# Kernel tuning notes

Hardware: AMD Instinct MI355X
Metric: run time of the kernel (lower is better)

## Reference

```python
import jax, jax.numpy as jnp
import numpy as np

B, S_SRC, S_TRG = 128, 512, 128
VIN, VOUT = 128, 128
E, H = 128, 256          # embed, encoder hidden
HD = 2 * H               # decoder hidden = 512 (concat of bi-dir encoder states)
DENC = 2 * H             # encoder output feature dim = 512


def setup_inputs() -> dict:
    key = jax.random.key(0)
    ks = jax.random.split(key, 20)
    g = lambda k, shape: (jax.random.normal(k, shape, jnp.float32) * 0.05)
    inp = {
        "src": jax.random.randint(ks[0], (B, S_SRC), 0, VIN, jnp.int32),
        "trg": jax.random.randint(ks[1], (B, S_TRG), 0, VOUT, jnp.int32),
        # encoder
        "enc_emb": g(ks[2], (VIN, E)),
        "enc_Wih_f": g(ks[3], (4 * H, E)),
        "enc_Whh_f": g(ks[4], (4 * H, H)),
        "enc_b_f": g(ks[5], (4 * H,)),
        "enc_Wih_b": g(ks[6], (4 * H, E)),
        "enc_Whh_b": g(ks[7], (4 * H, H)),
        "enc_b_b": g(ks[8], (4 * H,)),
        # decoder
        "dec_emb": g(ks[9], (VOUT, E)),
        "dec_Wih": g(ks[10], (4 * HD, E + DENC)),
        "dec_Whh": g(ks[11], (4 * HD, HD)),
        "dec_b": g(ks[12], (4 * HD,)),
        # attention: Linear(dec_hid + enc_dim -> HD), v: Linear(HD -> 1)
        "attn_W": g(ks[13], (HD + DENC, HD)),
        "attn_b": g(ks[14], (HD,)),
        "attn_v": g(ks[15], (HD,)),
        # output projection
        "out_W": g(ks[16], (HD, VOUT)),
        "out_b": g(ks[17], (VOUT,)),
    }
    return inp


def _lstm_cell(h, c, x, Wih, Whh, b):
    gates = x @ Wih.T + h @ Whh.T + b               # [B, 4H]
    i, f, gg, o = jnp.split(gates, 4, axis=-1)       # PyTorch gate order i,f,g,o
    i, f, o = jax.nn.sigmoid(i), jax.nn.sigmoid(f), jax.nn.sigmoid(o)
    c = f * c + i * jnp.tanh(gg)
    h = o * jnp.tanh(c)
    return h, c


def _lstm_scan(xs, Wih, Whh, b, reverse=False):
    # xs: [S, B, E] -> hs: [S, B, H] (time-aligned), plus final (h, c)
    Bn, Hn = xs.shape[1], Whh.shape[1]
    init = (jnp.zeros((Bn, Hn), xs.dtype), jnp.zeros((Bn, Hn), xs.dtype))
    def step(carry, x):
        h, c = _lstm_cell(carry[0], carry[1], x, Wih, Whh, b)
        return (h, c), h
    (h, c), hs = jax.lax.scan(step, init, xs, reverse=reverse)
    return hs, h, c


def reference(src, trg, enc_emb, enc_Wih_f, enc_Whh_f, enc_b_f,
              enc_Wih_b, enc_Whh_b, enc_b_b, dec_emb, dec_Wih, dec_Whh,
              dec_b, attn_W, attn_b, attn_v, out_W, out_b):
    # ----- encoder (bidirectional LSTM) -----
    emb = enc_emb[src]                                # [B, S, E]
    xs = jnp.swapaxes(emb, 0, 1)                      # [S, B, E]
    hs_f, hf, cf = _lstm_scan(xs, enc_Wih_f, enc_Whh_f, enc_b_f, reverse=False)
    hs_b, hb, cb = _lstm_scan(xs, enc_Wih_b, enc_Whh_b, enc_b_b, reverse=True)
    enc_out = jnp.swapaxes(jnp.concatenate([hs_f, hs_b], -1), 0, 1)  # [B, S, 2H]
    hidden = jnp.concatenate([hf, hb], -1)            # [B, HD]  (hidden.view(1,B,-1))
    cell = jnp.concatenate([cf, cb], -1)              # [B, HD]

    # attention linear split: energy = tanh([h, enc] @ W + b)
    Wh, We = attn_W[:HD], attn_W[HD:]
    enc_proj = jnp.einsum("bsd,de->bse", enc_out, We)  # [B, S, HD] precomputed

    def dec_step(carry, tok):
        h, c = carry
        e = jnp.tanh(h[:, None, :] @ Wh + enc_proj + attn_b)     # [B, S, HD]
        scores = jnp.einsum("bse,e->bs", e, attn_v)              # [B, S]
        aw = jax.nn.softmax(scores, axis=1)
        ctx = jnp.einsum("bs,bsd->bd", aw, enc_out)              # [B, DENC]
        x = jnp.concatenate([dec_emb[tok], ctx], -1)             # [B, E+DENC]
        h, c = _lstm_cell(h, c, x, dec_Wih, dec_Whh, dec_b)
        logits = h @ out_W + out_b                               # [B, VOUT]
        return (h, c), logits

    # teacher forcing (ratio=1.0): input at step t is trg[:, t-1], t = 1..T-1
    toks = jnp.swapaxes(trg[:, :-1], 0, 1)            # [T-1, B]
    _, logits = jax.lax.scan(dec_step, (hidden, cell), toks)
    logits = jnp.swapaxes(logits, 0, 1)               # [B, T-1, VOUT]
    outputs = jnp.concatenate(
        [jnp.zeros((src.shape[0], 1, VOUT), logits.dtype), logits], axis=1)
    return outputs
```

## Files before the change

kernel.cpp:

```cpp
#include <hip/hip_runtime.h>


typedef _Float16 f16;
typedef _Float16 half8 __attribute__((ext_vector_type(8)));
typedef float f32x4 __attribute__((ext_vector_type(4)));
typedef char char8v __attribute__((ext_vector_type(8)));

#define MFMA16(a, b, c) __builtin_amdgcn_mfma_f32_16x16x32_f16((a), (b), (c), 0, 0, 0)

#define PSCALE (2.5f / 127.f)
#define PINV   (127.f / 2.5f)

__device__ __forceinline__ float fsig(float x) {
    return __builtin_amdgcn_rcpf(1.f + __expf(-x));
}
__device__ __forceinline__ float ftanh(float x) {
    return 1.f - 2.f * __builtin_amdgcn_rcpf(1.f + __expf(2.f * x));
}
__device__ __forceinline__ int frag_idx(int m, int k, int KS) {
    return (((m >> 4) * KS + (k >> 5)) * 64 + (((k >> 3) & 3) * 16 + (m & 15))) * 8 + (k & 7);
}

__device__ __forceinline__ void lds_barrier() {
    asm volatile("s_waitcnt lgkmcnt(0)" ::: "memory");
    __builtin_amdgcn_sched_barrier(0);
    __builtin_amdgcn_s_barrier();
    __builtin_amdgcn_sched_barrier(0);
}

__global__ void k_zero(unsigned* __restrict__ s)
{
    for (int z = threadIdx.x; z < 4112; z += 256) s[z] = 0u;
}

__global__ __launch_bounds__(256) void k_prep(
    const float* __restrict__ attn_W, const float* __restrict__ out_W,
    const float* __restrict__ enc_emb,
    const float* __restrict__ wihf, const float* __restrict__ wihb,
    const float* __restrict__ whhf, const float* __restrict__ whhb,
    const float* __restrict__ dec_emb, const float* __restrict__ dec_wih,
    const float* __restrict__ dec_whh,
    f16* __restrict__ WhT_sw, f16* __restrict__ outWT_sw,
    f16* __restrict__ whhf_sw, f16* __restrict__ whhb_sw,
    f16* __restrict__ decwih_sw, f16* __restrict__ decwhh_sw,
    f16* __restrict__ WeT, f16* __restrict__ emb16,
    f16* __restrict__ wihf16, f16* __restrict__ wihb16,
    f16* __restrict__ decemb16, float* __restrict__ out)
{
    long i = (long)blockIdx.x * 256 + threadIdx.x;
    if (i >= 3784704L) return;
    long idx = i;
    if (idx < 262144) {
        int j = idx & 7, lane = (idx >> 3) & 63, c = lane & 15, q = lane >> 4;
        int ks = (idx >> 9) & 15, nt = idx >> 13;
        WhT_sw[idx] = (f16)attn_W[(ks * 32 + q * 8 + j) * 512 + nt * 16 + c];
        return;
    }
    idx -= 262144;
    if (idx < 65536) {
        int j = idx & 7, lane = (idx >> 3) & 63, c = lane & 15, q = lane >> 4;
        int ks = (idx >> 9) & 15, nt = idx >> 13;
        outWT_sw[idx] = (f16)out_W[(ks * 32 + q * 8 + j) * 128 + nt * 16 + c];
        return;
    }
    idx -= 65536;
    if (idx < 262144) {
        int j = idx & 7, lane = (idx >> 3) & 63, c = lane & 15, q = lane >> 4;
        int ks = (idx >> 9) & 7, nt = idx >> 12;
        whhf_sw[idx] = (f16)whhf[(nt * 16 + c) * 256 + ks * 32 + q * 8 + j];
        return;
    }
    idx -= 262144;
    if (idx < 262144) {
        int j = idx & 7, lane = (idx >> 3) & 63, c = lane & 15, q = lane >> 4;
        int ks = (idx >> 9) & 7, nt = idx >> 12;
        whhb_sw[idx] = (f16)whhb[(nt * 16 + c) * 256 + ks * 32 + q * 8 + j];
        return;
    }
    idx -= 262144;
    if (idx < 1310720) {
        int j = idx & 7, lane = (idx >> 3) & 63, c = lane & 15, q = lane >> 4;
        int r2 = idx >> 9; int ks = r2 % 20, nt = r2 / 20;
        decwih_sw[idx] = (f16)dec_wih[(nt * 16 + c) * 640 + ks * 32 + q * 8 + j];
        return;
    }
    idx -= 1310720;
    if (idx < 1048576) {
        int j = idx & 7, lane = (idx >> 3) & 63, c = lane & 15, q = lane >> 4;
        int ks = (idx >> 9) & 15, nt = idx >> 13;
        decwhh_sw[idx] = (f16)dec_whh[(nt * 16 + c) * 512 + ks * 32 + q * 8 + j];
        return;
    }
    idx -= 1048576;
    if (idx < 262144) { int e = idx >> 9, d = idx & 511; WeT[idx] = (f16)attn_W[(512 + d) * 512 + e]; return; }
    idx -= 262144;
    if (idx < 16384)  { emb16[idx] = (f16)enc_emb[idx]; return; }
    idx -= 16384;
    if (idx < 131072) { wihf16[idx] = (f16)wihf[idx]; return; }
    idx -= 131072;
    if (idx < 131072) { wihb16[idx] = (f16)wihb[idx]; return; }
    idx -= 131072;
    if (idx < 16384)  { decemb16[idx] = (f16)dec_emb[idx]; return; }
    idx -= 16384;
    if (idx < 16384)  { int b = idx >> 7, v = idx & 127; out[b * 16384 + v] = 0.f; return; }
}

__global__ __launch_bounds__(256) void k_vocab(
    const f16* __restrict__ emb, const f16* __restrict__ wihf,
    const f16* __restrict__ wihb, const float* __restrict__ bf_,
    const float* __restrict__ bb_, f16* __restrict__ xg_vocab)
{
    int bn = blockIdx.x;
    int tid = threadIdx.x, wave = tid >> 6, lane = tid & 63;
    int col = lane & 15, quad = lane >> 4;
    int wr = wave >> 1, wc = wave & 1;

    f32x4 acc[4][4] = {};
    for (int ks = 0; ks < 4; ++ks) {
        int k0 = ks * 32 + quad * 8;
        half8 a[4], bfr[4];
        for (int i = 0; i < 4; ++i)
            a[i] = *(const half8*)(emb + (wr * 64 + i * 16 + col) * 128 + k0);
        for (int j = 0; j < 4; ++j) {
            int n = bn * 128 + wc * 64 + j * 16 + col;
            const f16* wp = (n < 1024) ? (wihf + n * 128) : (wihb + (n - 1024) * 128);
            bfr[j] = *(const half8*)(wp + k0);
        }
        for (int i = 0; i < 4; ++i)
            for (int j = 0; j < 4; ++j)
                acc[i][j] = MFMA16(a[i], bfr[j], acc[i][j]);
    }
    for (int j = 0; j < 4; ++j) {
        int n = bn * 128 + wc * 64 + j * 16 + col;
        float bias = (n < 1024) ? bf_[n] : bb_[n - 1024];
        for (int i = 0; i < 4; ++i) {
            int vbase = wr * 64 + i * 16 + quad * 4;
            for (int r = 0; r < 4; ++r)
                xg_vocab[(vbase + r) * 2048 + n] = (f16)(acc[i][j][r] + bias);
        }
    }
}

__global__ __launch_bounds__(512, 1) void k_enc(
    const int* __restrict__ src, const f16* __restrict__ xg_vocab,
    const f16* __restrict__ whhf_sw, const f16* __restrict__ whhb_sw,
    f16* __restrict__ enc_out, f16* __restrict__ hdec0, float* __restrict__ c_ws)
{
    int blk = blockIdx.x;
    int dir = blk >> 3, bbase = (blk & 7) * 16;
    int tid = threadIdx.x, wave = tid >> 6, lane = tid & 63;
    int col = lane & 15, quad = lane >> 4;
    const f16* whh = dir ? whhb_sw : whhf_sw;

    __shared__ f16 hb[2][16][264];
    __shared__ f16 xvb[2][16][1032];
    __shared__ unsigned short stall[8192];

    for (int z = tid; z < 2 * 16 * 264; z += 512) ((f16*)hb)[z] = (f16)0.f;
    for (int z = tid; z < 8192; z += 512) stall[z] = (unsigned short)src[bbase * 512 + z];
    float cc[2][4] = {};

    half8 bst[16];
    #pragma unroll
    for (int nt = 0; nt < 2; ++nt)
        #pragma unroll
        for (int kk = 0; kk < 8; ++kk) {
            int tile = wave * 2 + nt;
            bst[nt * 8 + kk] = *(const half8*)(whh + ((tile * 8 + kk) * 64 + lane) * 8);
        }
    __syncthreads();

    int xrow = tid >> 7, xoff = (tid & 127) * 8;
    half8 xr[4];
    {
        int ts0 = dir ? 511 : 0;
        #pragma unroll
        for (int it = 0; it < 4; ++it) {
            int row = it * 4 + xrow;
            int tok = stall[row * 512 + ts0];
            xr[it] = *(const half8*)(xg_vocab + tok * 2048 + dir * 1024 + xoff);
        }
        #pragma unroll
        for (int it = 0; it < 4; ++it)
            *(half8*)(&xvb[0][it * 4 + xrow][xoff]) = xr[it];
    }
    __syncthreads();

    int ts_prev = 0;
    for (int t = 0; t < 512; ++t) {
        int ts = dir ? (511 - t) : t;
        int cur = t & 1, prv = cur ^ 1;

        if (t < 511) {
            int tsn = dir ? (510 - t) : (t + 1);
            #pragma unroll
            for (int it = 0; it < 4; ++it) {
                int row = it * 4 + xrow;
                int tok = stall[row * 512 + tsn];
                xr[it] = *(const half8*)(xg_vocab + tok * 2048 + dir * 1024 + xoff);
            }
        }

        if (t > 0) {
            int b = tid >> 5, seg = tid & 31;
            *(half8*)(enc_out + ((size_t)(bbase + b) * 512 + ts_prev) * 512 + dir * 256 + seg * 8) =
                *(const half8*)(&hb[prv][b][seg * 8]);
        }

        half8 a[8];
        #pragma unroll
        for (int kk = 0; kk < 8; ++kk)
            a[kk] = *(const half8*)(&hb[prv][col][kk * 32 + quad * 8]);

        f32x4 acc[4][2] = {};
        #pragma unroll
        for (int kk = 0; kk < 8; ++kk) {
            half8 bv[6];
            #pragma unroll
            for (int g = 1; g < 4; ++g)
                #pragma unroll
                for (int nt = 0; nt < 2; ++nt) {
                    int tile = g * 16 + wave * 2 + nt;
                    bv[(g - 1) * 2 + nt] =
                        *(const half8*)(whh + ((tile * 8 + kk) * 64 + lane) * 8);
                }
            #pragma unroll
            for (int nt = 0; nt < 2; ++nt)
                acc[0][nt] = MFMA16(a[kk], bst[nt * 8 + kk], acc[0][nt]);
            #pragma unroll
            for (int g = 1; g < 4; ++g)
                #pragma unroll
                for (int nt = 0; nt < 2; ++nt)
                    acc[g][nt] = MFMA16(a[kk], bv[(g - 1) * 2 + nt], acc[g][nt]);
        }

        #pragma unroll
        for (int nt = 0; nt < 2; ++nt) {
            int hcol = wave * 32 + nt * 16 + col;
            #pragma unroll
            for (int r = 0; r < 4; ++r) {
                int b = quad * 4 + r;
                float gi = (float)xvb[cur][b][0 * 256 + hcol] + acc[0][nt][r];
                float gf = (float)xvb[cur][b][1 * 256 + hcol] + acc[1][nt][r];
                float gg = (float)xvb[cur][b][2 * 256 + hcol] + acc[2][nt][r];
                float go = (float)xvb[cur][b][3 * 256 + hcol] + acc[3][nt][r];
                float ig = fsig(gi), fg = fsig(gf), g2 = ftanh(gg), og = fsig(go);
                float cv = fg * cc[nt][r] + ig * g2;
                cc[nt][r] = cv;
                float h = og * ftanh(cv);
                hb[cur][b][hcol] = (f16)h;
            }
        }

        if (t < 511) {
            #pragma unroll
            for (int it = 0; it < 4; ++it)
                *(half8*)(&xvb[prv][it * 4 + xrow][xoff]) = xr[it];
        }

        lds_barrier();
        ts_prev = ts;
    }

    {
        int b = tid >> 5, seg = tid & 31;
        *(half8*)(enc_out + ((size_t)(bbase + b) * 512 + ts_prev) * 512 + dir * 256 + seg * 8) =
            *(const half8*)(&hb[1][b][seg * 8]);
    }
    #pragma unroll
    for (int nt = 0; nt < 2; ++nt) {
        int hcol = wave * 32 + nt * 16 + col;
        #pragma unroll
        for (int r = 0; r < 4; ++r) {
            int b = quad * 4 + r;
            int m = bbase + b, k = dir * 256 + hcol;
            hdec0[frag_idx(m, k, 16)] = hb[1][b][hcol];
            c_ws[m * 512 + k] = cc[nt][r];
        }
    }
}

__global__ __launch_bounds__(256) void k_proj(
    const f16* __restrict__ enc_out, const f16* __restrict__ WeT,
    char* __restrict__ proj8)
{
    int blk = blockIdx.x;
    int bm = blk & 511, bn = blk >> 9;
    int tid = threadIdx.x, wave = tid >> 6, lane = tid & 63;
    int col = lane & 15, quad = lane >> 4;
    int wr = wave >> 1, wc = wave & 1;

    f32x4 acc[4][4] = {};
    for (int ks = 0; ks < 16; ++ks) {
        int k0 = ks * 32 + quad * 8;
        half8 a[4], bfr[4];
        for (int i = 0; i < 4; ++i) {
            int m = bm * 128 + wr * 64 + i * 16 + col;
            a[i] = *(const half8*)(enc_out + (size_t)m * 512 + k0);
        }
        for (int j = 0; j < 4; ++j) {
            int n = bn * 128 + wc * 64 + j * 16 + col;
            bfr[j] = *(const half8*)(WeT + n * 512 + k0);
        }
        for (int i = 0; i < 4; ++i)
            for (int j = 0; j < 4; ++j)
                acc[i][j] = MFMA16(a[i], bfr[j], acc[i][j]);
    }
    for (int j = 0; j < 4; ++j) {
        int n = bn * 128 + wc * 64 + j * 16 + col;
        for (int i = 0; i < 4; ++i) {
            int mbase = bm * 128 + wr * 64 + i * 16 + quad * 4;
            for (int r = 0; r < 4; ++r) {
                float v = acc[i][j][r] * PINV;
                int q = (int)rintf(v);
                q = (q > 127) ? 127 : ((q < -127) ? -127 : q);
                proj8[(size_t)(mbase + r) * 512 + n] = (char)q;
            }
        }
    }
}

__global__ __launch_bounds__(256) void k_qinit(
    const f16* __restrict__ h0_sw, const f16* __restrict__ WhT_sw,
    float* __restrict__ qpart)
{
    int j = blockIdx.x;
    int tid = threadIdx.x, wave = tid >> 6, lane = tid & 63;
    int col = lane & 15, quad = lane >> 4;
    half8 a[2];
    #pragma unroll
    for (int i = 0; i < 2; ++i)
        a[i] = *(const half8*)(h0_sw + (((wave * 2 + i) * 16 + j) * 64 + lane) * 8);
    for (int nt = 0; nt < 32; ++nt) {
        half8 bfr = *(const half8*)(WhT_sw + ((nt * 16 + j) * 64 + lane) * 8);
        f32x4 q0 = {}, q1 = {};
        q0 = MFMA16(a[0], bfr, q0);
        q1 = MFMA16(a[1], bfr, q1);
        #pragma unroll
        for (int r = 0; r < 4; ++r) {
            qpart[(j * 128 + wave * 32 + quad * 4 + r) * 512 + nt * 16 + col] = q0[r];
            qpart[(j * 128 + wave * 32 + 16 + quad * 4 + r) * 512 + nt * 16 + col] = q1[r];
        }
    }
}

__global__ __launch_bounds__(512, 2) void k_step(
    const char* __restrict__ proj8, const f16* __restrict__ enc_out,
    float* __restrict__ qpart, const float* __restrict__ attn_bp,
    const float* __restrict__ attn_vp, const int* __restrict__ trg,
    const f16* __restrict__ dec_emb, f16* __restrict__ x_sw,
    float* __restrict__ part_m, float* __restrict__ part_l,
    float* __restrict__ part_ctx, f16* __restrict__ hdec0,
    f16* __restrict__ hdec1, const f16* __restrict__ wih_sw,
    const f16* __restrict__ whh_sw, const float* __restrict__ dec_bp,
    float* __restrict__ c_ws, f16* __restrict__ hhist_sw,
    const f16* __restrict__ WhT_sw, unsigned* __restrict__ flags, int tt)
{
    int blk = blockIdx.x;
    int tid = threadIdx.x, wave = tid >> 6, lane = tid & 63;
    int col = lane & 15, quad = lane >> 4;

    __shared__ float q[512];
    __shared__ float sc[256];
    __shared__ float ctxred[8][512];
    __shared__ float wred[8], wred2[8];
    __shared__ f16 hsl[64][40];
    __shared__ float gm[64][2];
    __shared__ float gq[4][4][4][64];

    if (blk < 32) {
        int tg = tt - 1;
        if (tg >= 0) {
            int j = blk >> 1, mh = blk & 1;
            if (tid < 64) {
                int bb = mh * 64 + tid;
                float m0 = part_m[bb * 2 + 0], m1 = part_m[bb * 2 + 1];
                float l0 = part_l[bb * 2 + 0], l1 = part_l[bb * 2 + 1];
                float M = fmaxf(m0, m1);
                float g0 = __expf(m0 - M), g1 = __expf(m1 - M);
                float inv = 1.f / (g0 * l0 + g1 * l1);
                gm[tid][0] = g0 * inv;
                gm[tid][1] = g1 * inv;
            }
            __syncthreads();

            for (int io = 0; io < 64; io += 8) {
                float p0[8], p1[8];
                #pragma unroll
                for (int k = 0; k < 8; ++k) {
                    int bb = mh * 64 + io + k;
                    p0[k] = part_ctx[(size_t)(bb * 2 + 0) * 512 + tid];
                    p1[k] = part_ctx[(size_t)(bb * 2 + 1) * 512 + tid];
                }
                #pragma unroll
                for (int k = 0; k < 8; ++k) {
                    int lr = io + k, bb = mh * 64 + lr;
                    x_sw[frag_idx(bb, 128 + tid, 20)] =
                        (f16)(gm[lr][0] * p0[k] + gm[lr][1] * p1[k]);
                }
            }
            __syncthreads();

            const f16* hprev = (tg & 1) ? hdec1 : hdec0;
            f16* hnext = (tg & 1) ? hdec0 : hdec1;

            int h = wave >> 2, mw = wave & 3;
            int mtile = mh * 4 + mw;

            f32x4 acc[4] = {};
            for (int kg = 0; kg < 20; kg += 4) {
                half8 ag[4], bvg[4][4];
                #pragma unroll
                for (int kk = 0; kk < 4; ++kk) {
                    int ks = kg + kk;
                    ag[kk] = *(const half8*)(x_sw + ((mtile * 20 + ks) * 64 + lane) * 8);
                    #pragma unroll
                    for (int q2 = 0; q2 < 4; ++q2) {
                        int jt = h * 4 + q2, g = jt >> 1, u2 = jt & 1;
                        int ntile = g * 32 + j * 2 + u2;
                        bvg[kk][q2] = *(const half8*)(wih_sw + ((ntile * 20 + ks) * 64 + lane) * 8);
                    }
                }
                #pragma unroll
                for (int kk = 0; kk < 4; ++kk)
                    #pragma unroll
                    for (int q2 = 0; q2 < 4; ++q2)
                        acc[q2] = MFMA16(ag[kk], bvg[kk][q2], acc[q2]);
            }
            for (int kg = 0; kg < 16; kg += 4) {
                half8 ag[4], bvg[4][4];
                #pragma unroll
                for (int kk = 0; kk < 4; ++kk) {
                    int ks2 = kg + kk;
                    ag[kk] = *(const half8*)(hprev + ((mtile * 16 + ks2) * 64 + lane) * 8);
                    #pragma unroll
                    for (int q2 = 0; q2 < 4; ++q2) {
                        int jt = h * 4 + q2, g = jt >> 1, u2 = jt & 1;
                        int ntile = g * 32 + j * 2 + u2;
                        bvg[kk][q2] = *(const half8*)(whh_sw + ((ntile * 16 + ks2) * 64 + lane) * 8);
                    }
                }
                #pragma unroll
                for (int kk = 0; kk < 4; ++kk)
                    #pragma unroll
                    for (int q2 = 0; q2 < 4; ++q2)
                        acc[q2] = MFMA16(ag[kk], bvg[kk][q2], acc[q2]);
            }

            float bias[4];
            #pragma unroll
            for (int q2 = 0; q2 < 4; ++q2) {
                int jt = h * 4 + q2, g = jt >> 1, u2 = jt & 1;
                bias[q2] = dec_bp[g * 512 + j * 32 + u2 * 16 + col];
            }
            if (h == 1) {
                #pragma unroll
                for (int q2 = 0; q2 < 4; ++q2)
                    #pragma unroll
                    for (int r = 0; r < 4; ++r)
                        gq[mw][q2][r][lane] = acc[q2][r] + bias[q2];
            }
            __syncthreads();

            if (h == 0) {
                #pragma unroll
                for (int r = 0; r < 4; ++r) {
                    int lb = mw * 16 + quad * 4 + r;
                    int bb = mh * 64 + lb;
                    #pragma unroll
                    for (int u2 = 0; u2 < 2; ++u2) {
                        int hl = u2 * 16 + col, hcol = j * 32 + hl;
                        float gi = acc[0 + u2][r] + bias[0 + u2];
                        float gf = acc[2 + u2][r] + bias[2 + u2];
                        float gg = gq[mw][0 + u2][r][lane];
                        float go = gq[mw][2 + u2][r][lane];
                        float ig = fsig(gi), fg = fsig(gf), g2 = ftanh(gg), og = fsig(go);
                        float cv = fg * c_ws[bb * 512 + hcol] + ig * g2;
                        c_ws[bb * 512 + hcol] = cv;
                        float hv = og * ftanh(cv);
                        f16 h16 = (f16)hv;
                        int fidx = frag_idx(bb, hcol, 16);
                        hnext[fidx] = h16;
                        hhist_sw[tg * 65536 + fidx] = h16;
                        hsl[lb][hl] = h16;
                    }
                }
            }
            __syncthreads();

            half8 aq = *(const half8*)(&hsl[mw * 16 + col][quad * 8]);
            for (int ng = 0; ng < 4; ++ng) {
                half8 bq[4];
                #pragma unroll
                for (int k = 0; k < 4; ++k) {
                    int nt = h * 16 + ng * 4 + k;
                    bq[k] = *(const half8*)(WhT_sw + ((nt * 16 + j) * 64 + lane) * 8);
                }
                #pragma unroll
                for (int k = 0; k < 4; ++k) {
                    int nt = h * 16 + ng * 4 + k;
                    f32x4 q0 = {};
                    q0 = MFMA16(aq, bq[k], q0);
                    #pragma unroll
                    for (int r = 0; r < 4; ++r)
                        qpart[(j * 128 + mh * 64 + mw * 16 + quad * 4 + r) * 512 + nt * 16 + col] = q0[r];
                }
            }

            __syncthreads();
            if (tid == 0)
                __hip_atomic_store(flags + blk * 16, (unsigned)tt,
                                   __ATOMIC_RELEASE, __HIP_MEMORY_SCOPE_AGENT);
        }
        return;
    }

    int ab = blk - 32;
    int b = ab >> 1, sh = ab & 1;
    int sbase = sh * 256;

    float vreg[8];
    #pragma unroll
    for (int u = 0; u < 8; ++u) vreg[u] = attn_vp[lane * 8 + u];
    float abias = attn_bp[tid];

    char8v p0[8];
    #pragma unroll
    for (int z = 0; z < 8; ++z) {
        int sl = z * 8 + wave;
        p0[z] = *(const char8v*)(proj8 + ((size_t)b * 512 + sbase + sl) * 512 + lane * 8);
    }

    if (tt > 0) {
        if (wave == 0) {
            for (;;) {
                unsigned v = (lane < 32)
                    ? __hip_atomic_load(flags + lane * 16, __ATOMIC_RELAXED,
                                        __HIP_MEMORY_SCOPE_AGENT)
                    : (unsigned)tt;
                if (__ballot(v >= (unsigned)tt) == ~0ull) break;
                __builtin_amdgcn_s_sleep(8);
            }
            if (lane == 0)
                (void)__hip_atomic_load(flags, __ATOMIC_ACQUIRE,
                                        __HIP_MEMORY_SCOPE_AGENT);
        }
        __syncthreads();
    }

    {
        float s = abias;
        #pragma unroll
        for (int jj = 0; jj < 16; ++jj) s += qpart[(jj * 128 + b) * 512 + tid];
        q[tid] = s;
    }
    __syncthreads();

    float qreg[8];
    #pragma unroll
    for (int u = 0; u < 8; ++u) qreg[u] = q[lane * 8 + u];

    #pragma unroll
    for (int z = 0; z < 8; ++z) {
        int sl = z * 8 + wave;
        float part = 0.f;
        #pragma unroll
        for (int u = 0; u < 8; ++u)
            part += vreg[u] * ftanh(fmaf((float)p0[z][u], PSCALE, qreg[u]));
        #pragma unroll
        for (int o = 32; o; o >>= 1) part += __shfl_xor(part, o);
        if (lane == 0) sc[sl] = part;
    }
    for (int ib = 1; ib < 4; ++ib) {
        char8v p[8];
        #pragma unroll
        for (int z = 0; z < 8; ++z) {
            int sl = (ib * 8 + z) * 8 + wave;
            p[z] = *(const char8v*)(proj8 + ((size_t)b * 512 + sbase + sl) * 512 + lane * 8);
        }
        #pragma unroll
        for (int z = 0; z < 8; ++z) {
            int sl = (ib * 8 + z) * 8 + wave;
            float part = 0.f;
            #pragma unroll
            for (int u = 0; u < 8; ++u)
                part += vreg[u] * ftanh(fmaf((float)p[z][u], PSCALE, qreg[u]));
            #pragma unroll
            for (int o = 32; o; o >>= 1) part += __shfl_xor(part, o);
            if (lane == 0) sc[sl] = part;
        }
    }
    __syncthreads();

    float s0 = (tid < 256) ? sc[tid] : -__builtin_inff();
    float mv = s0;
    #pragma unroll
    for (int o = 32; o; o >>= 1) mv = fmaxf(mv, __shfl_xor(mv, o));
    if (lane == 0) wred[wave] = mv;
    __syncthreads();
    float M = wred[0];
    #pragma unroll
    for (int w = 1; w < 8; ++w) M = fmaxf(M, wred[w]);
    float e0 = (tid < 256) ? __expf(s0 - M) : 0.f;
    if (tid < 256) sc[tid] = e0;
    float sm = e0;
    #pragma unroll
    for (int o = 32; o; o >>= 1) sm += __shfl_xor(sm, o);
    if (lane == 0) wred2[wave] = sm;
    __syncthreads();
    float lsum = wred2[0];
    #pragma unroll
    for (int w = 1; w < 8; ++w) lsum += wred2[w];

    float a8[8] = {};
    for (int ib = 0; ib < 4; ++ib) {
        half8 ev[8];
        float wgt[8];
        #pragma unroll
        for (int z = 0; z < 8; ++z) {
            int sl = (ib * 8 + z) * 8 + wave;
            ev[z] = *(const half8*)(enc_out + ((size_t)b * 512 + sbase + sl) * 512 + lane * 8);
            wgt[z] = sc[sl];
        }
        #pragma unroll
        for (int z = 0; z < 8; ++z)
            #pragma unroll
            for (int u = 0; u < 8; ++u) a8[u] += wgt[z] * (float)ev[z][u];
    }
    #pragma unroll
    for (int u = 0; u < 8; ++u) ctxred[wave][lane * 8 + u] = a8[u];
    __syncthreads();
    float cp = 0.f;
    #pragma unroll
    for (int w = 0; w < 8; ++w) cp += ctxred[w][tid];
    part_ctx[(size_t)ab * 512 + tid] = cp;
    if (tid == 0) { part_m[ab] = M; part_l[ab] = lsum; }

    if (sh == 0 && tid < 128) {
        int tok = trg[b * 128 + tt];
        x_sw[frag_idx(b, tid, 20)] = dec_emb[tok * 128 + tid];
    }
}

__global__ __launch_bounds__(256) void k_gates(
    f16* __restrict__ x_sw, const f16* __restrict__ hprev_sw,
    const f16* __restrict__ wih_sw, const f16* __restrict__ whh_sw,
    const float* __restrict__ dec_b, float* __restrict__ c_ws,
    f16* __restrict__ hnext_sw, f16* __restrict__ hhist_sw,
    const f16* __restrict__ WhT_sw, float* __restrict__ qpart,
    const float* __restrict__ part_m, const float* __restrict__ part_l,
    const float* __restrict__ part_ctx, int t)
{
    int jb = blockIdx.x;
    int j = jb >> 1, mh = jb & 1;
    int tid = threadIdx.x, wave = tid >> 6, lane = tid & 63;
    int col = lane & 15, quad = lane >> 4;
    __shared__ f16 hsl[64][40];
    __shared__ float gm[64][2];

    if (tid < 64) {
        int bb = mh * 64 + tid;
        float m0 = part_m[bb * 2 + 0], m1 = part_m[bb * 2 + 1];
        float l0 = part_l[bb * 2 + 0], l1 = part_l[bb * 2 + 1];
        float M = fmaxf(m0, m1);
        float g0 = __expf(m0 - M), g1 = __expf(m1 - M);
        float inv = 1.f / (g0 * l0 + g1 * l1);
        gm[tid][0] = g0 * inv;
        gm[tid][1] = g1 * inv;
    }
    __syncthreads();
    for (int z = tid; z < 32768; z += 256) {
        int lr = z >> 9, d = z & 511;
        int bb = mh * 64 + lr;
        float c = gm[lr][0] * part_ctx[(size_t)(bb * 2 + 0) * 512 + d]
                + gm[lr][1] * part_ctx[(size_t)(bb * 2 + 1) * 512 + d];
        x_sw[frag_idx(bb, 128 + d, 20)] = (f16)c;
    }
    __syncthreads();

    f32x4 acc[8] = {};
    for (int ks = 0; ks < 36; ++ks) {
        int mtile = mh * 4 + wave;
        half8 a = (ks < 20)
            ? *(const half8*)(x_sw + ((mtile * 20 + ks) * 64 + lane) * 8)
            : *(const half8*)(hprev_sw + ((mtile * 16 + (ks - 20)) * 64 + lane) * 8);
        half8 bv[8];
        #pragma unroll
        for (int jt = 0; jt < 8; ++jt) {
            int g = jt >> 1, u2 = jt & 1;
            int ntile = g * 32 + j * 2 + u2;
            bv[jt] = (ks < 20)
                ? *(const half8*)(wih_sw + ((ntile * 20 + ks) * 64 + lane) * 8)
                : *(const half8*)(whh_sw + ((ntile * 16 + (ks - 20)) * 64 + lane) * 8);
        }
        #pragma unroll
        for (int jt = 0; jt < 8; ++jt)
            acc[jt] = MFMA16(a, bv[jt], acc[jt]);
    }
    float bias[8];
    #pragma unroll
    for (int jt = 0; jt < 8; ++jt) {
        int g = jt >> 1, u2 = jt & 1;
        bias[jt] = dec_b[g * 512 + j * 32 + u2 * 16 + col];
    }
    #pragma unroll
    for (int r = 0; r < 4; ++r) {
        int lb = wave * 16 + quad * 4 + r;
        int bb = mh * 64 + lb;
        #pragma unroll
        for (int u2 = 0; u2 < 2; ++u2) {
            int hl = u2 * 16 + col, hcol = j * 32 + hl;
            float gi = acc[0 + u2][r] + bias[0 + u2];
            float gf = acc[2 + u2][r] + bias[2 + u2];
            float gg = acc[4 + u2][r] + bias[4 + u2];
            float go = acc[6 + u2][r] + bias[6 + u2];
            float ig = fsig(gi), fg = fsig(gf), g2 = ftanh(gg), og = fsig(go);
            float cv = fg * c_ws[bb * 512 + hcol] + ig * g2;
            c_ws[bb * 512 + hcol] = cv;
            float h = og * ftanh(cv);
            f16 h16 = (f16)h;
            int fidx = frag_idx(bb, hcol, 16);
            hnext_sw[fidx] = h16;
            hhist_sw[t * 65536 + fidx] = h16;
            hsl[lb][hl] = h16;
        }
    }
    half8 aq = *(const half8*)(&hsl[wave * 16 + col][quad * 8]);
    for (int nt = 0; nt < 32; ++nt) {
        half8 bq = *(const half8*)(WhT_sw + ((nt * 16 + j) * 64 + lane) * 8);
        f32x4 q0 = {};
        q0 = MFMA16(aq, bq, q0);
        #pragma unroll
        for (int r = 0; r < 4; ++r)
            qpart[(j * 128 + mh * 64 + wave * 16 + quad * 4 + r) * 512 + nt * 16 + col] = q0[r];
    }
}

__global__ __launch_bounds__(256) void k_logits(
    const f16* __restrict__ hhist_sw, const f16* __restrict__ outWT_sw,
    const float* __restrict__ out_b, float* __restrict__ out)
{
    int bt = blockIdx.x;
    int tid = threadIdx.x, wave = tid >> 6, lane = tid & 63;
    int col = lane & 15, quad = lane >> 4;
    f32x4 acc[2][8] = {};
    for (int ks = 0; ks < 16; ++ks) {
        half8 a[2];
        #pragma unroll
        for (int i = 0; i < 2; ++i)
            a[i] = *(const half8*)(hhist_sw + bt * 65536 + (((wave * 2 + i) * 16 + ks) * 64 + lane) * 8);
        half8 bv[8];
        #pragma unroll
        for (int jt = 0; jt < 8; ++jt)
            bv[jt] = *(const half8*)(outWT_sw + ((jt * 16 + ks) * 64 + lane) * 8);
        #pragma unroll
        for (int jt = 0; jt < 8; ++jt) {
            acc[0][jt] = MFMA16(a[0], bv[jt], acc[0][jt]);
            acc[1][jt] = MFMA16(a[1], bv[jt], acc[1][jt]);
        }
    }
    #pragma unroll
    for (int jt = 0; jt < 8; ++jt) {
        float bias = out_b[jt * 16 + col];
        #pragma unroll
        for (int i = 0; i < 2; ++i)
            #pragma unroll
            for (int r = 0; r < 4; ++r) {
                int br = wave * 32 + i * 16 + quad * 4 + r;
                out[br * 16384 + (bt + 1) * 128 + jt * 16 + col] = acc[i][jt][r] + bias;
            }
    }
}

extern "C" void kernel_launch(void* const* d_in, const int* in_sizes, int n_in,
                              void* d_out, int out_size, void* d_ws, size_t ws_size,
                              hipStream_t stream)
{
    (void)in_sizes; (void)n_in; (void)out_size;
    if (ws_size < 130000000) return;

    const int*   src     = (const int*)d_in[0];
    const int*   trg     = (const int*)d_in[1];
    const float* enc_emb = (const float*)d_in[2];
    const float* wihf    = (const float*)d_in[3];
    const float* whhf    = (const float*)d_in[4];
    const float* bf_     = (const float*)d_in[5];
    const float* wihb    = (const float*)d_in[6];
    const float* whhb    = (const float*)d_in[7];
    const float* bb_     = (const float*)d_in[8];
    const float* dec_emb = (const float*)d_in[9];
    const float* dec_wih = (const float*)d_in[10];
    const float* dec_whh = (const float*)d_in[11];
    const float* dec_b   = (const float*)d_in[12];
    const float* attn_W  = (const float*)d_in[13];
    const float* attn_b  = (const float*)d_in[14];
    const float* attn_v  = (const float*)d_in[15];
    const float* out_W   = (const float*)d_in[16];
    const float* out_b   = (const float*)d_in[17];
    float* out = (float*)d_out;

    char* p = (char*)d_ws;
    auto carve = [&](size_t n) { char* r = p; p += ((n + 255) & ~(size_t)255); return r; };
    f16*   enc_out   = (f16*)  carve(67108864);
    char*  proj8     = (char*) carve(33554432);
    f16*   WhT_sw    = (f16*)  carve(524288);
    f16*   WeT       = (f16*)  carve(524288);
    f16*   outWT_sw  = (f16*)  carve(131072);
    f16*   emb16     = (f16*)  carve(32768);
    f16*   wihf16    = (f16*)  carve(262144);
    f16*   wihb16    = (f16*)  carve(262144);
    f16*   whhf_sw   = (f16*)  carve(524288);
    f16*   whhb_sw   = (f16*)  carve(524288);
    f16*   decemb16  = (f16*)  carve(32768);
    f16*   decwih_sw = (f16*)  carve(2621440);
    f16*   decwhh_sw = (f16*)  carve(2097152);
    float* qpart     = (float*)carve(4194304);
    f16*   hdec0     = (f16*)  carve(131072);
    f16*   hdec1     = (f16*)  carve(131072);
    float* c_ws      = (float*)carve(262144);
    f16*   x_sw      = (f16*)  carve(163840);
    f16*   hhist_sw  = (f16*)  carve(16646144);
    f16*   xg_vocab  = (f16*)  carve(524288);
    float* part_m    = (float*)carve(2048);
    float* part_l    = (float*)carve(2048);
    float* part_ctx  = (float*)carve(524288);
    unsigned* flagsv = (unsigned*)carve(16448);

    k_zero<<<1, 256, 0, stream>>>(flagsv);
    k_prep<<<14784, 256, 0, stream>>>(attn_W, out_W, enc_emb, wihf, wihb, whhf, whhb,
                                      dec_emb, dec_wih, dec_whh,
                                      WhT_sw, outWT_sw, whhf_sw, whhb_sw,
                                      decwih_sw, decwhh_sw, WeT, emb16,
                                      wihf16, wihb16, decemb16, out);
    k_vocab<<<16, 256, 0, stream>>>(emb16, wihf16, wihb16, bf_, bb_, xg_vocab);
    k_enc<<<16, 512, 0, stream>>>(src, xg_vocab, whhf_sw, whhb_sw, enc_out, hdec0, c_ws);
    k_proj<<<2048, 256, 0, stream>>>(enc_out, WeT, proj8);
    k_qinit<<<16, 256, 0, stream>>>(hdec0, WhT_sw, qpart);

    for (int tt = 0; tt < 127; ++tt)
        k_step<<<288, 512, 0, stream>>>(proj8, enc_out, qpart, attn_b, attn_v,
                                        trg, decemb16, x_sw, part_m, part_l,
                                        part_ctx, hdec0, hdec1, decwih_sw,
                                        decwhh_sw, dec_b, c_ws, hhist_sw,
                                        WhT_sw, flagsv, tt);
    k_gates<<<32, 256, 0, stream>>>(x_sw, hdec0, decwih_sw, decwhh_sw, dec_b,
                                    c_ws, hdec1, hhist_sw, WhT_sw, qpart,
                                    part_m, part_l, part_ctx, 126);

    k_logits<<<127, 256, 0, stream>>>(hhist_sw, outWT_sw, out_b, out);
}
```

Baseline: 10.94 ms.

## Fuse per-step decoder launches into one persistent kernel with flag handshakes

Replaces the 127 per-timestep k_step launches plus the trailing k_gates launch with a single persistent k_decode kernel that loops over time internally. Gate blocks and attention blocks sync through global release/acquire flag counters in both directions, and shared memory is unioned to shrink the footprint so more blocks fit per CU. This removes launch overhead and the implicit grid-wide barriers between steps. The cost is spin-wait polling and a deadlock risk if all 288 blocks are not co-resident.

```diff
diff --git a/kernel.cpp b/kernel.cpp
--- a/kernel.cpp
+++ b/kernel.cpp
@@ -30,7 +30,7 @@
 
 __global__ void k_zero(unsigned* __restrict__ s)
 {
-    for (int z = threadIdx.x; z < 4112; z += 256) s[z] = 0u;
+    for (int z = threadIdx.x; z < 8192; z += 256) s[z] = 0u;
 }
 
 __global__ __launch_bounds__(256) void k_prep(
@@ -344,7 +344,7 @@
     }
 }
 
-__global__ __launch_bounds__(512, 2) void k_step(
+__global__ __launch_bounds__(512, 4) void k_decode(
     const char* __restrict__ proj8, const f16* __restrict__ enc_out,
     float* __restrict__ qpart, const float* __restrict__ attn_bp,
     const float* __restrict__ attn_vp, const int* __restrict__ trg,
@@ -354,24 +354,53 @@
     f16* __restrict__ hdec1, const f16* __restrict__ wih_sw,
     const f16* __restrict__ whh_sw, const float* __restrict__ dec_bp,
     float* __restrict__ c_ws, f16* __restrict__ hhist_sw,
-    const f16* __restrict__ WhT_sw, unsigned* __restrict__ flags, int tt)
+    const f16* __restrict__ WhT_sw, unsigned* __restrict__ flags)
 {
     int blk = blockIdx.x;
     int tid = threadIdx.x, wave = tid >> 6, lane = tid & 63;
     int col = lane & 15, quad = lane >> 4;
 
-    __shared__ float q[512];
-    __shared__ float sc[256];
-    __shared__ float ctxred[8][512];
-    __shared__ float wred[8], wred2[8];
-    __shared__ f16 hsl[64][40];
-    __shared__ float gm[64][2];
-    __shared__ float gq[4][4][4][64];
+    __shared__ union SU {
+        struct { float q[512]; float sc[256]; float ctxred[8][512];
+                 float wred[8], wred2[8]; } att;
+        struct { f16 hsl[64][40]; float gm[64][2]; float gq[4][4][4][64]; } gat;
+    } su;
 
     if (blk < 32) {
-        int tg = tt - 1;
-        if (tg >= 0) {
-            int j = blk >> 1, mh = blk & 1;
+        int j = blk >> 1, mh = blk & 1;
+        int h = wave >> 2, mw = wave & 3;
+        int mtile = mh * 4 + mw;
+        float bias[4];
+        #pragma unroll
+        for (int q2 = 0; q2 < 4; ++q2) {
+            int jt = h * 4 + q2, g = jt >> 1, u2 = jt & 1;
+            bias[q2] = dec_bp[g * 512 + j * 32 + u2 * 16 + col];
+        }
+
+        for (int tt = 0; tt < 127; ++tt) {
+            {
+                unsigned tgt = (unsigned)(tt + 1);
+                if (wave == 0) {
+                    for (;;) {
+                        unsigned v0 = __hip_atomic_load(flags + 2048 + (lane +   0) * 16,
+                                                        __ATOMIC_RELAXED, __HIP_MEMORY_SCOPE_AGENT);
+                        unsigned v1 = __hip_atomic_load(flags + 2048 + (lane +  64) * 16,
+                                                        __ATOMIC_RELAXED, __HIP_MEMORY_SCOPE_AGENT);
+                        unsigned v2 = __hip_atomic_load(flags + 2048 + (lane + 128) * 16,
+                                                        __ATOMIC_RELAXED, __HIP_MEMORY_SCOPE_AGENT);
+                        unsigned v3 = __hip_atomic_load(flags + 2048 + (lane + 192) * 16,
+                                                        __ATOMIC_RELAXED, __HIP_MEMORY_SCOPE_AGENT);
+                        bool ok = (v0 >= tgt) && (v1 >= tgt) && (v2 >= tgt) && (v3 >= tgt);
+                        if (__ballot(ok) == ~0ull) break;
+                        __builtin_amdgcn_s_sleep(8);
+                    }
+                    if (lane == 0)
+                        (void)__hip_atomic_load(flags + 2048, __ATOMIC_ACQUIRE,
+                                                __HIP_MEMORY_SCOPE_AGENT);
+                }
+                __syncthreads();
+            }
+
             if (tid < 64) {
                 int bb = mh * 64 + tid;
                 float m0 = part_m[bb * 2 + 0], m1 = part_m[bb * 2 + 1];
@@ -379,11 +408,10 @@
                 float M = fmaxf(m0, m1);
                 float g0 = __expf(m0 - M), g1 = __expf(m1 - M);
                 float inv = 1.f / (g0 * l0 + g1 * l1);
-                gm[tid][0] = g0 * inv;
-                gm[tid][1] = g1 * inv;
+                su.gat.gm[tid][0] = g0 * inv;
+                su.gat.gm[tid][1] = g1 * inv;
             }
             __syncthreads();
-
             for (int io = 0; io < 64; io += 8) {
                 float p0[8], p1[8];
                 #pragma unroll
@@ -396,16 +424,13 @@
                 for (int k = 0; k < 8; ++k) {
                     int lr = io + k, bb = mh * 64 + lr;
                     x_sw[frag_idx(bb, 128 + tid, 20)] =
-                        (f16)(gm[lr][0] * p0[k] + gm[lr][1] * p1[k]);
+                        (f16)(su.gat.gm[lr][0] * p0[k] + su.gat.gm[lr][1] * p1[k]);
                 }
             }
             __syncthreads();
 
-            const f16* hprev = (tg & 1) ? hdec1 : hdec0;
-            f16* hnext = (tg & 1) ? hdec0 : hdec1;
-
-            int h = wave >> 2, mw = wave & 3;
-            int mtile = mh * 4 + mw;
+            const f16* hprev = (tt & 1) ? hdec1 : hdec0;
+            f16* hnext = (tt & 1) ? hdec0 : hdec1;
 
             f32x4 acc[4] = {};
             for (int kg = 0; kg < 20; kg += 4) {
@@ -447,18 +472,12 @@
                         acc[q2] = MFMA16(ag[kk], bvg[kk][q2], acc[q2]);
             }
 
-            float bias[4];
-            #pragma unroll
-            for (int q2 = 0; q2 < 4; ++q2) {
-                int jt = h * 4 + q2, g = jt >> 1, u2 = jt & 1;
-                bias[q2] = dec_bp[g * 512 + j * 32 + u2 * 16 + col];
-            }
             if (h == 1) {
                 #pragma unroll
                 for (int q2 = 0; q2 < 4; ++q2)
                     #pragma unroll
                     for (int r = 0; r < 4; ++r)
-                        gq[mw][q2][r][lane] = acc[q2][r] + bias[q2];
+                        su.gat.gq[mw][q2][r][lane] = acc[q2][r] + bias[q2];
             }
             __syncthreads();
 
@@ -472,8 +491,8 @@
                         int hl = u2 * 16 + col, hcol = j * 32 + hl;
                         float gi = acc[0 + u2][r] + bias[0 + u2];
                         float gf = acc[2 + u2][r] + bias[2 + u2];
-                        float gg = gq[mw][0 + u2][r][lane];
-                        float go = gq[mw][2 + u2][r][lane];
+                        float gg = su.gat.gq[mw][0 + u2][r][lane];
+                        float go = su.gat.gq[mw][2 + u2][r][lane];
                         float ig = fsig(gi), fg = fsig(gf), g2 = ftanh(gg), og = fsig(go);
                         float cv = fg * c_ws[bb * 512 + hcol] + ig * g2;
                         c_ws[bb * 512 + hcol] = cv;
@@ -481,14 +500,14 @@
                         f16 h16 = (f16)hv;
                         int fidx = frag_idx(bb, hcol, 16);
                         hnext[fidx] = h16;
-                        hhist_sw[tg * 65536 + fidx] = h16;
-                        hsl[lb][hl] = h16;
+                        hhist_sw[tt * 65536 + fidx] = h16;
+                        su.gat.hsl[lb][hl] = h16;
                     }
                 }
             }
             __syncthreads();
 
-            half8 aq = *(const half8*)(&hsl[mw * 16 + col][quad * 8]);
+            half8 aq = *(const half8*)(&su.gat.hsl[mw * 16 + col][quad * 8]);
             for (int ng = 0; ng < 4; ++ng) {
                 half8 bq[4];
                 #pragma unroll
@@ -509,7 +528,7 @@
 
             __syncthreads();
             if (tid == 0)
-                __hip_atomic_store(flags + blk * 16, (unsigned)tt,
+                __hip_atomic_store(flags + blk * 16, (unsigned)(tt + 1),
                                    __ATOMIC_RELEASE, __HIP_MEMORY_SCOPE_AGENT);
         }
         return;
@@ -524,215 +543,145 @@
     for (int u = 0; u < 8; ++u) vreg[u] = attn_vp[lane * 8 + u];
     float abias = attn_bp[tid];
 
-    char8v p0[8];
-    #pragma unroll
-    for (int z = 0; z < 8; ++z) {
-        int sl = z * 8 + wave;
-        p0[z] = *(const char8v*)(proj8 + ((size_t)b * 512 + sbase + sl) * 512 + lane * 8);
-    }
-
-    if (tt > 0) {
-        if (wave == 0) {
-            for (;;) {
-                unsigned v = (lane < 32)
-                    ? __hip_atomic_load(flags + lane * 16, __ATOMIC_RELAXED,
-                                        __HIP_MEMORY_SCOPE_AGENT)
-                    : (unsigned)tt;
-                if (__ballot(v >= (unsigned)tt) == ~0ull) break;
-                __builtin_amdgcn_s_sleep(8);
-            }
-            if (lane == 0)
-                (void)__hip_atomic_load(flags, __ATOMIC_ACQUIRE,
-                                        __HIP_MEMORY_SCOPE_AGENT);
+    for (int tt = 0; tt < 127; ++tt) {
+        char8v pA[8], pB[8];
+        #pragma unroll
+        for (int z = 0; z < 8; ++z) {
+            int sl = z * 8 + wave;
+            pA[z] = *(const char8v*)(proj8 + ((size_t)b * 512 + sbase + sl) * 512 + lane * 8);
+        }
+        #pragma unroll
+        for (int z = 0; z < 8; ++z) {
+            int sl = (8 + z) * 8 + wave;
+            pB[z] = *(const char8v*)(proj8 + ((size_t)b * 512 + sbase + sl) * 512 + lane * 8);
+        }
+
+        if (tt > 0) {
+            if (wave == 0) {
+                unsigned tgt = (unsigned)tt;
+                for (;;) {
+                    unsigned v = (lane < 32)
+                        ? __hip_atomic_load(flags + lane * 16, __ATOMIC_RELAXED,
+                                            __HIP_MEMORY_SCOPE_AGENT)
+                        : tgt;
+                    if (__ballot(v >= tgt) == ~0ull) break;
+                    __builtin_amdgcn_s_sleep(8);
+                }
+                if (lane == 0)
+                    (void)__hip_atomic_load(flags, __ATOMIC_ACQUIRE,
+                                            __HIP_MEMORY_SCOPE_AGENT);
+            }
+            __syncthreads();
+        }
+
+        {
+            float s = abias;
+            #pragma unroll
+            for (int jj = 0; jj < 16; ++jj) s += qpart[(jj * 128 + b) * 512 + tid];
+            su.att.q[tid] = s;
         }
         __syncthreads();
-    }
-
-    {
-        float s = abias;
-        #pragma unroll
-        for (int jj = 0; jj < 16; ++jj) s += qpart[(jj * 128 + b) * 512 + tid];
-        q[tid] = s;
-    }
-    __syncthreads();
-
-    float qreg[8];
-    #pragma unroll
-    for (int u = 0; u < 8; ++u) qreg[u] = q[lane * 8 + u];
-
-    #pragma unroll
-    for (int z = 0; z < 8; ++z) {
-        int sl = z * 8 + wave;
-        float part = 0.f;
-        #pragma unroll
-        for (int u = 0; u < 8; ++u)
-            part += vreg[u] * ftanh(fmaf((float)p0[z][u], PSCALE, qreg[u]));
-        #pragma unroll
-        for (int o = 32; o; o >>= 1) part += __shfl_xor(part, o);
-        if (lane == 0) sc[sl] = part;
-    }
-    for (int ib = 1; ib < 4; ++ib) {
-        char8v p[8];
+
+        float qreg[8];
+        #pragma unroll
+        for (int u = 0; u < 8; ++u) qreg[u] = su.att.q[lane * 8 + u];
+
         #pragma unroll
         for (int z = 0; z < 8; ++z) {
-            int sl = (ib * 8 + z) * 8 + wave;
-            p[z] = *(const char8v*)(proj8 + ((size_t)b * 512 + sbase + sl) * 512 + lane * 8);
+            int sl = z * 8 + wave;
+            float part = 0.f;
+            #pragma unroll
+            for (int u = 0; u < 8; ++u)
+                part += vreg[u] * ftanh(fmaf((float)pA[z][u], PSCALE, qreg[u]));
+            #pragma unroll
+            for (int o = 32; o; o >>= 1) part += __shfl_xor(part, o);
+            if (lane == 0) su.att.sc[sl] = part;
         }
         #pragma unroll
         for (int z = 0; z < 8; ++z) {
-            int sl = (ib * 8 + z) * 8 + wave;
+            int sl = (8 + z) * 8 + wave;
             float part = 0.f;
             #pragma unroll
             for (int u = 0; u < 8; ++u)
-                part += vreg[u] * ftanh(fmaf((float)p[z][u], PSCALE, qreg[u]));
+                part += vreg[u] * ftanh(fmaf((float)pB[z][u], PSCALE, qreg[u]));
             #pragma unroll
             for (int o = 32; o; o >>= 1) part += __shfl_xor(part, o);
-            if (lane == 0) sc[sl] = part;
-        }
-    }
-    __syncthreads();
-
-    float s0 = (tid < 256) ? sc[tid] : -__builtin_inff();
-    float mv = s0;
-    #pragma unroll
-    for (int o = 32; o; o >>= 1) mv = fmaxf(mv, __shfl_xor(mv, o));
-    if (lane == 0) wred[wave] = mv;
-    __syncthreads();
-    float M = wred[0];
-    #pragma unroll
-    for (int w = 1; w < 8; ++w) M = fmaxf(M, wred[w]);
-    float e0 = (tid < 256) ? __expf(s0 - M) : 0.f;
-    if (tid < 256) sc[tid] = e0;
-    float sm = e0;
-    #pragma unroll
-    for (int o = 32; o; o >>= 1) sm += __shfl_xor(sm, o);
-    if (lane == 0) wred2[wave] = sm;
-    __syncthreads();
-    float lsum = wred2[0];
-    #pragma unroll
-    for (int w = 1; w < 8; ++w) lsum += wred2[w];
-
-    float a8[8] = {};
-    for (int ib = 0; ib < 4; ++ib) {
-        half8 ev[8];
-        float wgt[8];
-        #pragma unroll
-        for (int z = 0; z < 8; ++z) {
-            int sl = (ib * 8 + z) * 8 + wave;
-            ev[z] = *(const half8*)(enc_out + ((size_t)b * 512 + sbase + sl) * 512 + lane * 8);
-            wgt[z] = sc[sl];
-        }
-        #pragma unroll
-        for (int z = 0; z < 8; ++z)
-            #pragma unroll
-            for (int u = 0; u < 8; ++u) a8[u] += wgt[z] * (float)ev[z][u];
-    }
-    #pragma unroll
-    for (int u = 0; u < 8; ++u) ctxred[wave][lane * 8 + u] = a8[u];
-    __syncthreads();
-    float cp = 0.f;
-    #pragma unroll
-    for (int w = 0; w < 8; ++w) cp += ctxred[w][tid];
-    part_ctx[(size_t)ab * 512 + tid] = cp;
-    if (tid == 0) { part_m[ab] = M; part_l[ab] = lsum; }
-
-    if (sh == 0 && tid < 128) {
-        int tok = trg[b * 128 + tt];
-        x_sw[frag_idx(b, tid, 20)] = dec_emb[tok * 128 + tid];
-    }
-}
-
-__global__ __launch_bounds__(256) void k_gates(
-    f16* __restrict__ x_sw, const f16* __restrict__ hprev_sw,
-    const f16* __restrict__ wih_sw, const f16* __restrict__ whh_sw,
-    const float* __restrict__ dec_b, float* __restrict__ c_ws,
-    f16* __restrict__ hnext_sw, f16* __restrict__ hhist_sw,
-    const f16* __restrict__ WhT_sw, float* __restrict__ qpart,
-    const float* __restrict__ part_m, const float* __restrict__ part_l,
-    const float* __restrict__ part_ctx, int t)
-{
-    int jb = blockIdx.x;
-    int j = jb >> 1, mh = jb & 1;
-    int tid = threadIdx.x, wave = tid >> 6, lane = tid & 63;
-    int col = lane & 15, quad = lane >> 4;
-    __shared__ f16 hsl[64][40];
-    __shared__ float gm[64][2];
-
-    if (tid < 64) {
-        int bb = mh * 64 + tid;
-        float m0 = part_m[bb * 2 + 0], m1 = part_m[bb * 2 + 1];
-        float l0 = part_l[bb * 2 + 0], l1 = part_l[bb * 2 + 1];
-        float M = fmaxf(m0, m1);
-        float g0 = __expf(m0 - M), g1 = __expf(m1 - M);
-        float inv = 1.f / (g0 * l0 + g1 * l1);
-        gm[tid][0] = g0 * inv;
-        gm[tid][1] = g1 * inv;
-    }
-    __syncthreads();
-    for (int z = tid; z < 32768; z += 256) {
-        int lr = z >> 9, d = z & 511;
-        int bb = mh * 64 + lr;
-        float c = gm[lr][0] * part_ctx[(size_t)(bb * 2 + 0) * 512 + d]
-                + gm[lr][1] * part_ctx[(size_t)(bb * 2 + 1) * 512 + d];
-        x_sw[frag_idx(bb, 128 + d, 20)] = (f16)c;
-    }
-    __syncthreads();
-
-    f32x4 acc[8] = {};
-    for (int ks = 0; ks < 36; ++ks) {
-        int mtile = mh * 4 + wave;
-        half8 a = (ks < 20)
-            ? *(const half8*)(x_sw + ((mtile * 20 + ks) * 64 + lane) * 8)
-            : *(const half8*)(hprev_sw + ((mtile * 16 + (ks - 20)) * 64 + lane) * 8);
-        half8 bv[8];
-        #pragma unroll
-        for (int jt = 0; jt < 8; ++jt) {
-            int g = jt >> 1, u2 = jt & 1;
-            int ntile = g * 32 + j * 2 + u2;
-            bv[jt] = (ks < 20)
-                ? *(const half8*)(wih_sw + ((ntile * 20 + ks) * 64 + lane) * 8)
-                : *(const half8*)(whh_sw + ((ntile * 16 + (ks - 20)) * 64 + lane) * 8);
-        }
-        #pragma unroll
-        for (int jt = 0; jt < 8; ++jt)
-            acc[jt] = MFMA16(a, bv[jt], acc[jt]);
-    }
-    float bias[8];
-    #pragma unroll
-    for (int jt = 0; jt < 8; ++jt) {
-        int g = jt >> 1, u2 = jt & 1;
-        bias[jt] = dec_b[g * 512 + j * 32 + u2 * 16 + col];
-    }
-    #pragma unroll
-    for (int r = 0; r < 4; ++r) {
-        int lb = wave * 16 + quad * 4 + r;
-        int bb = mh * 64 + lb;
-        #pragma unroll
-        for (int u2 = 0; u2 < 2; ++u2) {
-            int hl = u2 * 16 + col, hcol = j * 32 + hl;
-            float gi = acc[0 + u2][r] + bias[0 + u2];
-            float gf = acc[2 + u2][r] + bias[2 + u2];
-            float gg = acc[4 + u2][r] + bias[4 + u2];
-            float go = acc[6 + u2][r] + bias[6 + u2];
-            float ig = fsig(gi), fg = fsig(gf), g2 = ftanh(gg), og = fsig(go);
-            float cv = fg * c_ws[bb * 512 + hcol] + ig * g2;
-            c_ws[bb * 512 + hcol] = cv;
-            float h = og * ftanh(cv);
-            f16 h16 = (f16)h;
-            int fidx = frag_idx(bb, hcol, 16);
-            hnext_sw[fidx] = h16;
-            hhist_sw[t * 65536 + fidx] = h16;
-            hsl[lb][hl] = h16;
-        }
-    }
-    half8 aq = *(const half8*)(&hsl[wave * 16 + col][quad * 8]);
-    for (int nt = 0; nt < 32; ++nt) {
-        half8 bq = *(const half8*)(WhT_sw + ((nt * 16 + j) * 64 + lane) * 8);
-        f32x4 q0 = {};
-        q0 = MFMA16(aq, bq, q0);
-        #pragma unroll
-        for (int r = 0; r < 4; ++r)
-            qpart[(j * 128 + mh * 64 + wave * 16 + quad * 4 + r) * 512 + nt * 16 + col] = q0[r];
+            if (lane == 0) su.att.sc[sl] = part;
+        }
+        for (int ib = 2; ib < 4; ++ib) {
+            char8v p[8];
+            #pragma unroll
+            for (int z = 0; z < 8; ++z) {
+                int sl = (ib * 8 + z) * 8 + wave;
+                p[z] = *(const char8v*)(proj8 + ((size_t)b * 512 + sbase + sl) * 512 + lane * 8);
+            }
+            #pragma unroll
+            for (int z = 0; z < 8; ++z) {
+                int sl = (ib * 8 + z) * 8 + wave;
+                float part = 0.f;
+                #pragma unroll
+                for (int u = 0; u < 8; ++u)
+                    part += vreg[u] * ftanh(fmaf((float)p[z][u], PSCALE, qreg[u]));
+                #pragma unroll
+                for (int o = 32; o; o >>= 1) part += __shfl_xor(part, o);
+                if (lane == 0) su.att.sc[sl] = part;
+            }
+        }
+        __syncthreads();
+
+        float s0 = (tid < 256) ? su.att.sc[tid] : -__builtin_inff();
+        float mv = s0;
+        #pragma unroll
+        for (int o = 32; o; o >>= 1) mv = fmaxf(mv, __shfl_xor(mv, o));
+        if (lane == 0) su.att.wred[wave] = mv;
+        __syncthreads();
+        float M = su.att.wred[0];
+        #pragma unroll
+        for (int w = 1; w < 8; ++w) M = fmaxf(M, su.att.wred[w]);
+        float e0 = (tid < 256) ? __expf(s0 - M) : 0.f;
+        if (tid < 256) su.att.sc[tid] = e0;
+        float sm = e0;
+        #pragma unroll
+        for (int o = 32; o; o >>= 1) sm += __shfl_xor(sm, o);
+        if (lane == 0) su.att.wred2[wave] = sm;
+        __syncthreads();
+        float lsum = su.att.wred2[0];
+        #pragma unroll
+        for (int w = 1; w < 8; ++w) lsum += su.att.wred2[w];
+
+        float a8[8] = {};
+        for (int ib = 0; ib < 4; ++ib) {
+            half8 ev[8];
+            float wgt[8];
+            #pragma unroll
+            for (int z = 0; z < 8; ++z) {
+                int sl = (ib * 8 + z) * 8 + wave;
+                ev[z] = *(const half8*)(enc_out + ((size_t)b * 512 + sbase + sl) * 512 + lane * 8);
+                wgt[z] = su.att.sc[sl];
+            }
+            #pragma unroll
+            for (int z = 0; z < 8; ++z)
+                #pragma unroll
+                for (int u = 0; u < 8; ++u) a8[u] += wgt[z] * (float)ev[z][u];
+        }
+        #pragma unroll
+        for (int u = 0; u < 8; ++u) su.att.ctxred[wave][lane * 8 + u] = a8[u];
+        __syncthreads();
+        float cp = 0.f;
+        #pragma unroll
+        for (int w = 0; w < 8; ++w) cp += su.att.ctxred[w][tid];
+        part_ctx[(size_t)ab * 512 + tid] = cp;
+        if (tid == 0) { part_m[ab] = M; part_l[ab] = lsum; }
+
+        if (sh == 0 && tid < 128) {
+            int tok = trg[b * 128 + tt];
+            x_sw[frag_idx(b, tid, 20)] = dec_emb[tok * 128 + tid];
+        }
+
+        __syncthreads();
+        if (tid == 0)
+            __hip_atomic_store(flags + 2048 + ab * 16, (unsigned)(tt + 1),
+                               __ATOMIC_RELEASE, __HIP_MEMORY_SCOPE_AGENT);
     }
 }
 
@@ -824,7 +773,7 @@
     float* part_m    = (float*)carve(2048);
     float* part_l    = (float*)carve(2048);
     float* part_ctx  = (float*)carve(524288);
-    unsigned* flagsv = (unsigned*)carve(16448);
+    unsigned* flagsv = (unsigned*)carve(32768);
 
     k_zero<<<1, 256, 0, stream>>>(flagsv);
     k_prep<<<14784, 256, 0, stream>>>(attn_W, out_W, enc_emb, wihf, wihb, whhf, whhb,
@@ -837,15 +786,11 @@
     k_proj<<<2048, 256, 0, stream>>>(enc_out, WeT, proj8);
     k_qinit<<<16, 256, 0, stream>>>(hdec0, WhT_sw, qpart);
 
-    for (int tt = 0; tt < 127; ++tt)
-        k_step<<<288, 512, 0, stream>>>(proj8, enc_out, qpart, attn_b, attn_v,
-                                        trg, decemb16, x_sw, part_m, part_l,
-                                        part_ctx, hdec0, hdec1, decwih_sw,
-                                        decwhh_sw, dec_b, c_ws, hhist_sw,
-                                        WhT_sw, flagsv, tt);
-    k_gates<<<32, 256, 0, stream>>>(x_sw, hdec0, decwih_sw, decwhh_sw, dec_b,
-                                    c_ws, hdec1, hhist_sw, WhT_sw, qpart,
-                                    part_m, part_l, part_ctx, 126);
+    k_decode<<<288, 512, 0, stream>>>(proj8, enc_out, qpart, attn_b, attn_v,
+                                      trg, decemb16, x_sw, part_m, part_l,
+                                      part_ctx, hdec0, hdec1, decwih_sw,
+                                      decwhh_sw, dec_b, c_ws, hhist_sw,
+                                      WhT_sw, flagsv);
 
     k_logits<<<127, 256, 0, stream>>>(hhist_sw, outWT_sw, out_b, out);
 }
```

Measured after the change: 32.68 ms. 2.99x slower.
